# Optimization experiments

Hardware: AMD Instinct MI355X
Metric: run time of the kernel (lower is better)

Reference implementation:

```python
import jax, jax.numpy as jnp
import numpy as np
from jax.ops import segment_sum

N_NODES = 100000


def _gcn_norm(src, dst, n):
    # add self-loops, compute symmetric normalization deg^-1/2 * deg^-1/2
    loop = jnp.arange(n, dtype=src.dtype)
    src_sl = jnp.concatenate([src, loop])
    dst_sl = jnp.concatenate([dst, loop])
    deg = segment_sum(jnp.ones_like(src_sl, dtype=jnp.float32), dst_sl, num_segments=n)
    dinv = jnp.where(deg > 0, jax.lax.rsqrt(deg), 0.0)
    norm = dinv[src_sl] * dinv[dst_sl]  # [E+N]
    return src_sl, dst_sl, norm


def _gcn_conv(x, W, b, src_sl, dst_sl, norm, n):
    h = x @ W                              # [N, out]  dense GEMM first (smaller msg dim)
    msg = h[src_sl] * norm[:, None]        # [E+N, out]
    out = segment_sum(msg, dst_sl, num_segments=n)
    return out + b


def setup_inputs() -> dict:
    key = jax.random.key(0)
    k1, k2, k3, k4, k5 = jax.random.split(key, 5)
    x = jax.random.normal(k1, (N_NODES, 400), dtype=jnp.float32)
    edge_index = jax.random.randint(k2, (2, 3200000), 0, N_NODES, dtype=jnp.int64)
    batch = jnp.zeros((N_NODES,), dtype=jnp.int64)
    # Glorot-style init like PyG GCNConv
    W1 = jax.random.normal(k3, (400, 128), dtype=jnp.float32) * (1.0 / np.sqrt(400))
    b1 = jnp.zeros((128,), dtype=jnp.float32)
    W2 = jax.random.normal(k4, (128, 128), dtype=jnp.float32) * (1.0 / np.sqrt(128))
    b2 = jnp.zeros((128,), dtype=jnp.float32)
    return {"x": x, "edge_index": edge_index, "batch": batch,
            "W1": W1, "b1": b1, "W2": W2, "b2": b2}


def reference(x, edge_index, batch, W1, b1, W2, b2):
    n = x.shape[0]
    src, dst = edge_index[0], edge_index[1]
    src_sl, dst_sl, norm = _gcn_norm(src, dst, n)
    h = jax.nn.relu(_gcn_conv(x, W1, b1, src_sl, dst_sl, norm, n))
    h = jax.nn.relu(_gcn_conv(h, W2, b2, src_sl, dst_sl, norm, n))
    return h
```

## Files before the change

### kernel.cpp

```cpp
#include <hip/hip_runtime.h>


#define NBMAX 1024
#define HB    512
#define CAPB  4608
#define TSLOG 13

using u16 = unsigned short;
using u32 = unsigned int;
typedef __attribute__((ext_vector_type(8))) short short8;
typedef __attribute__((ext_vector_type(4))) float f32x4;

__device__ __forceinline__ u16 f2bf(float f) {
    u32 u = __float_as_uint(f);
    u += 0x7fffu + ((u >> 16) & 1u);
    return (u16)(u >> 16);
}
__device__ __forceinline__ u32 pack2(float a, float b) {
    return (u32)f2bf(a) | ((u32)f2bf(b) << 16);
}
__device__ __forceinline__ float bflo(u32 u) { return __uint_as_float(u << 16); }
__device__ __forceinline__ float bfhi(u32 u) { return __uint_as_float(u & 0xffff0000u); }


__global__ __launch_bounds__(256) void k_init_bcur(u32* bcur, int NB) {
    int b = blockIdx.x * 256 + threadIdx.x;
    if (b < NB) bcur[b] = (u32)b * CAPB;
}

__global__ __launch_bounds__(256) void k_scatter(const int* __restrict__ src,
                                                 const int* __restrict__ dst,
                                                 u32* __restrict__ bcur,
                                                 u32* __restrict__ ebuf,
                                                 int E, int NB) {
    __shared__ u32 hist[NBMAX];
    __shared__ u32 base[NBMAX];
    const int tid = threadIdx.x;
    for (int i = tid; i < NB; i += 256) hist[i] = 0u;
    __syncthreads();
    const int chunk = (E + gridDim.x - 1) / gridDim.x;
    const int e0 = blockIdx.x * chunk;
    const int e1 = min(E, e0 + chunk);
    for (int i = e0 + tid; i < e1; i += 256)
        atomicAdd(&hist[dst[i] >> 7], 1u);
    __syncthreads();
    for (int i = tid; i < NB; i += 256) {
        const u32 c = hist[i];
        base[i] = c ? atomicAdd(&bcur[i], c) : 0u;
    }
    __syncthreads();
    for (int i = tid; i < NB; i += 256) hist[i] = 0u;
    __syncthreads();
    for (int i = e0 + tid; i < e1; i += 256) {
        const int s = src[i];
        const int d = dst[i];
        const int b = d >> 7;
        const u32 loc = atomicAdd(&hist[b], 1u);
        ebuf[base[b] + loc] = ((u32)(d & 127) << 17) | (u32)s;
    }
}

__global__ __launch_bounds__(256) void k_csr_build(const u32* __restrict__ ebuf,
                                                   const u32* __restrict__ bcur,
                                                   int* __restrict__ rowbeg,
                                                   u16* __restrict__ deg16,
                                                   float* __restrict__ dinv,
                                                   int* __restrict__ csr_s,
                                                   int N, int NB) {
    __shared__ u32 cnt[2048];
    __shared__ u32 scan[2048];
    __shared__ u32 cur[2048];
    __shared__ u32 bsum[256];
    const int tid = threadIdx.x;
    const int b = blockIdx.x;
    const int r0 = b * CAPB;
    const int r1 = (int)bcur[b];

    for (int i = tid; i < 2048; i += 256) cnt[i] = 0u;
    __syncthreads();
    for (int i = r0 + tid; i < r1; i += 256) {
        const u32 e = ebuf[i];
        const u32 key = ((e >> 17) << 4) | ((e & 0x1FFFFu) >> TSLOG);
        atomicAdd(&cnt[key], 1u);
    }
    __syncthreads();

    const int i8 = tid * 8;
    u32 pre[8];
    u32 run = 0;
#pragma unroll
    for (int j = 0; j < 8; ++j) { pre[j] = run; run += cnt[i8 + j]; }
    bsum[tid] = run;
    __syncthreads();
    for (int off = 1; off < 256; off <<= 1) {
        u32 v = bsum[tid];
        u32 add = (tid >= off) ? bsum[tid - off] : 0u;
        __syncthreads();
        bsum[tid] = v + add;
        __syncthreads();
    }
    const u32 excl = bsum[tid] - run;
#pragma unroll
    for (int j = 0; j < 8; ++j) {
        const u32 x = excl + pre[j];
        scan[i8 + j] = x;
        cur[i8 + j] = x;
    }
    __syncthreads();

    if (tid < 128) {
        const u32 beg  = scan[tid * 16];
        const u32 endv = (tid == 127) ? (u32)(r1 - r0) : scan[(tid + 1) * 16];
        const u32 dg   = endv - beg;
        const int node = b * 128 + tid;
        if (node < N) {
            rowbeg[node] = r0 + (int)beg;
            deg16[node]  = (u16)dg;
            dinv[node]   = rsqrtf((float)(dg + 1u));
        }
    }
    __syncthreads();

    for (int i = r0 + tid; i < r1; i += 256) {
        const u32 e = ebuf[i];
        const u32 sr = e & 0x1FFFFu;
        const u32 key = ((e >> 17) << 4) | (sr >> TSLOG);
        const u32 p = atomicAdd(&cur[key], 1u);
        csr_s[r0 + (int)p] = (int)sr;
    }
}

__global__ __launch_bounds__(256) void k_wprep(const float* __restrict__ W,
                                               u16* __restrict__ Wt,
                                               int K, int KP) {
    int idx = blockIdx.x * 256 + threadIdx.x;
    if (idx >= 128 * KP) return;
    int n = idx / KP, k = idx - n * KP;
    Wt[idx] = (k < K) ? f2bf(W[(size_t)k * 128 + n]) : (u16)0;
}

template <int ABF>
__global__ __launch_bounds__(512) void k_gemm_mfma(
        const void* __restrict__ Aptr,
        const u16* __restrict__ Wt,
        const float* __restrict__ dinv,
        u16* __restrict__ H, int M, int K, int KP) {
    __shared__ u16 smem[16384];
    u16* As = smem;
    u16* Bs = smem + 128 * 64;

    const int tid = threadIdx.x;
    const int row0 = blockIdx.x * 128;
    const int wid = tid >> 6;
    const int lane = tid & 63;
    const int wm = wid >> 2, wn = wid & 3;
    const int l15 = lane & 15, lg = lane >> 4;
    const int lr7 = l15 & 7;

    const int arow = tid >> 2;
    const int achk = tid & 3;
    const int grow = row0 + arow;
    const int ar7 = arow & 7;
    const int s0 = (achk * 2) ^ ar7;
    const int s1 = (achk * 2 + 1) ^ ar7;

    float4 ar0, ar1, ar2, ar3;
    uint4  au0, au1;
    uint4  bu0, bu1;

    auto load_tile = [&](int kt) {
        const int k0 = kt * 64 + achk * 16;
        if (ABF) {
            if (grow < M) {
                const u16* ap = (const u16*)Aptr + (size_t)grow * K + k0;
                au0 = *reinterpret_cast<const uint4*>(ap);
                au1 = *reinterpret_cast<const uint4*>(ap + 8);
            } else {
                au0 = make_uint4(0, 0, 0, 0);
                au1 = make_uint4(0, 0, 0, 0);
            }
        } else {
            if (grow < M && k0 < K) {
                const float* ap = (const float*)Aptr + (size_t)grow * K + k0;
                ar0 = *reinterpret_cast<const float4*>(ap);
                ar1 = *reinterpret_cast<const float4*>(ap + 4);
                ar2 = *reinterpret_cast<const float4*>(ap + 8);
                ar3 = *reinterpret_cast<const float4*>(ap + 12);
            } else {
                ar0 = ar1 = ar2 = ar3 = make_float4(0.f, 0.f, 0.f, 0.f);
            }
        }
        const u16* wp = Wt + (size_t)arow * KP + k0;
        bu0 = *reinterpret_cast<const uint4*>(wp);
        bu1 = *reinterpret_cast<const uint4*>(wp + 8);
    };

    auto store_tile = [&]() {
        uint4 w0, w1;
        if (ABF) {
            w0 = au0; w1 = au1;
        } else {
            w0.x = pack2(ar0.x, ar0.y); w0.y = pack2(ar0.z, ar0.w);
            w0.z = pack2(ar1.x, ar1.y); w0.w = pack2(ar1.z, ar1.w);
            w1.x = pack2(ar2.x, ar2.y); w1.y = pack2(ar2.z, ar2.w);
            w1.z = pack2(ar3.x, ar3.y); w1.w = pack2(ar3.z, ar3.w);
        }
        u16* ad = As + arow * 64;
        *reinterpret_cast<uint4*>(ad + s0 * 8) = w0;
        *reinterpret_cast<uint4*>(ad + s1 * 8) = w1;
        u16* bd = Bs + arow * 64;
        *reinterpret_cast<uint4*>(bd + s0 * 8) = bu0;
        *reinterpret_cast<uint4*>(bd + s1 * 8) = bu1;
    };

    f32x4 acc[4][2];
#pragma unroll
    for (int i = 0; i < 4; ++i)
#pragma unroll
        for (int j = 0; j < 2; ++j)
            acc[i][j] = (f32x4){0.f, 0.f, 0.f, 0.f};

    const int NT = KP >> 6;
    load_tile(0);
    for (int kt = 0; kt < NT; ++kt) {
        __syncthreads();
        store_tile();
        __syncthreads();
        if (kt + 1 < NT) load_tile(kt + 1);
#pragma unroll
        for (int sub = 0; sub < 2; ++sub) {
            const int slot = ((sub * 4 + lg) ^ lr7) * 8;
            short8 af[4], bf[2];
#pragma unroll
            for (int i = 0; i < 4; ++i)
                af[i] = *reinterpret_cast<const short8*>(
                    As + (wm * 64 + i * 16 + l15) * 64 + slot);
#pragma unroll
            for (int j = 0; j < 2; ++j)
                bf[j] = *reinterpret_cast<const short8*>(
                    Bs + (wn * 32 + j * 16 + l15) * 64 + slot);
#pragma unroll
            for (int i = 0; i < 4; ++i)
#pragma unroll
                for (int j = 0; j < 2; ++j)
                    acc[i][j] = __builtin_amdgcn_mfma_f32_16x16x32_bf16(
                        af[i], bf[j], acc[i][j], 0, 0, 0);
        }
    }

    const int CSTR = 136;
    __syncthreads();
#pragma unroll
    for (int half = 0; half < 2; ++half) {
        if (wm == half) {
#pragma unroll
            for (int i = 0; i < 4; ++i)
#pragma unroll
                for (int r = 0; r < 4; ++r) {
                    const int gr = row0 + half * 64 + i * 16 + lg * 4 + r;
                    const float dv = (gr < M) ? dinv[gr] : 0.f;
#pragma unroll
                    for (int j = 0; j < 2; ++j)
                        smem[(i * 16 + lg * 4 + r) * CSTR + wn * 32 + j * 16 + l15] =
                            f2bf(acc[i][j][r] * dv);
                }
        }
        __syncthreads();
        {
            const int rr = tid >> 3;
            const int cc = (tid & 7) * 16;
            const int gr = row0 + half * 64 + rr;
            if (gr < M) {
                const u16* cp = smem + rr * CSTR + cc;
                uint4 q0 = *reinterpret_cast<const uint4*>(cp);
                uint4 q1 = *reinterpret_cast<const uint4*>(cp + 8);
                uint4* hp = reinterpret_cast<uint4*>(H + (size_t)gr * 128 + cc);
                hp[0] = q0; hp[1] = q1;
            }
        }
        __syncthreads();
    }
}

template <int OUTBF>
__global__ __launch_bounds__(256) void k_gather(const int* __restrict__ rowbeg,
                                                const u16* __restrict__ deg16,
                                                const float* __restrict__ dinv,
                                                const int* __restrict__ csr_s,
                                                const u16* __restrict__ H,
                                                const float* __restrict__ bias,
                                                void* __restrict__ outp, int N) {
    const int t = threadIdx.x;
    const int node = blockIdx.x * 16 + (t >> 4);
    if (node >= N) return;
    const int lane = t & 15;
    const int c8 = lane * 8;

    const uint4 hv = *reinterpret_cast<const uint4*>(H + (size_t)node * 128 + c8);
    float acc0 = bflo(hv.x), acc1 = bfhi(hv.x);
    float acc2 = bflo(hv.y), acc3 = bfhi(hv.y);
    float acc4 = bflo(hv.z), acc5 = bfhi(hv.z);
    float acc6 = bflo(hv.w), acc7 = bfhi(hv.w);

    const int beg = rowbeg[node];
    const int end = beg + (int)deg16[node];
    for (int r = beg; r < end; r += 16) {
        const int cntc = min(16, end - r);
        int sv = (lane < cntc) ? csr_s[r + lane] : 0;
        for (int j = 0; j < cntc; ++j) {
            const int s = __shfl(sv, j, 16);
            const uint4 x = *reinterpret_cast<const uint4*>(H + (size_t)s * 128 + c8);
            acc0 += bflo(x.x); acc1 += bfhi(x.x);
            acc2 += bflo(x.y); acc3 += bfhi(x.y);
            acc4 += bflo(x.z); acc5 += bfhi(x.z);
            acc6 += bflo(x.w); acc7 += bfhi(x.w);
        }
    }

    const float dv = dinv[node];
    const float4 b0 = *reinterpret_cast<const float4*>(bias + c8);
    const float4 b1 = *reinterpret_cast<const float4*>(bias + c8 + 4);
    const float r0 = fmaxf(fmaf(acc0, dv, b0.x), 0.f);
    const float r1 = fmaxf(fmaf(acc1, dv, b0.y), 0.f);
    const float r2 = fmaxf(fmaf(acc2, dv, b0.z), 0.f);
    const float r3 = fmaxf(fmaf(acc3, dv, b0.w), 0.f);
    const float r4 = fmaxf(fmaf(acc4, dv, b1.x), 0.f);
    const float r5 = fmaxf(fmaf(acc5, dv, b1.y), 0.f);
    const float r6 = fmaxf(fmaf(acc6, dv, b1.z), 0.f);
    const float r7 = fmaxf(fmaf(acc7, dv, b1.w), 0.f);

    if (OUTBF) {
        uint4 q;
        q.x = pack2(r0, r1); q.y = pack2(r2, r3);
        q.z = pack2(r4, r5); q.w = pack2(r6, r7);
        u16* op = (u16*)outp + (size_t)node * 128 + c8;
        *reinterpret_cast<uint4*>(op) = q;
    } else {
        float* op = (float*)outp + (size_t)node * 128 + c8;
        *reinterpret_cast<float4*>(op)     = make_float4(r0, r1, r2, r3);
        *reinterpret_cast<float4*>(op + 4) = make_float4(r4, r5, r6, r7);
    }
}


extern "C" void kernel_launch(void* const* d_in, const int* in_sizes, int n_in,
                              void* d_out, int out_size, void* d_ws, size_t ws_size,
                              hipStream_t stream) {
    const float* x  = (const float*)d_in[0];
    const int*   ei = (const int*)d_in[1];
    const float* W1 = (const float*)d_in[3];
    const float* b1 = (const float*)d_in[4];
    const float* W2 = (const float*)d_in[5];
    const float* b2 = (const float*)d_in[6];
    float* out = (float*)d_out;

    const int N = in_sizes[0] / 400;
    const int E = in_sizes[1] / 2;
    const int* src = ei;
    const int* dst = ei + E;
    const int NB = (N + 127) >> 7;
    const int KP1 = 448;
    const int KP2 = 128;

    char* ws = (char*)d_ws;
    size_t off = 0;
    auto alloc = [&](size_t bytes) {
        void* p = ws + off;
        off = (off + bytes + 255) & ~(size_t)255;
        return p;
    };
    u32*   bcur   = (u32*)alloc((size_t)NB * 4);
    int*   rowbeg = (int*)alloc((size_t)N * 4);
    u16*   deg16  = (u16*)alloc((size_t)N * 2);
    float* dinv   = (float*)alloc((size_t)N * 4);
    int*   csr_s  = (int*)alloc((size_t)NB * CAPB * 4);
    u32*   ebuf   = (u32*)alloc((size_t)NB * CAPB * 4);
    u16*   hs     = (u16*)alloc((size_t)N * 128 * 2);
    u16*   abf    = (u16*)alloc((size_t)N * 128 * 2);
    u16*   Wt1    = (u16*)alloc((size_t)128 * KP1 * 2);
    u16*   Wt2    = (u16*)alloc((size_t)128 * KP2 * 2);

    const int nb_gm = (N + 127) / 128;
    const int nb_g  = (N + 15) / 16;

    k_wprep<<<(128 * KP1 + 255) / 256, 256, 0, stream>>>(W1, Wt1, 400, KP1);
    k_wprep<<<(128 * KP2 + 255) / 256, 256, 0, stream>>>(W2, Wt2, 128, KP2);

    k_init_bcur<<<(NB + 255) / 256, 256, 0, stream>>>(bcur, NB);
    k_scatter<<<HB, 256, 0, stream>>>(src, dst, bcur, ebuf, E, NB);
    k_csr_build<<<NB, 256, 0, stream>>>(ebuf, bcur, rowbeg, deg16, dinv, csr_s, N, NB);

    k_gemm_mfma<0><<<nb_gm, 512, 0, stream>>>(x, Wt1, dinv, hs, N, 400, KP1);
    k_gather<1><<<nb_g, 256, 0, stream>>>(rowbeg, deg16, dinv, csr_s, hs, b1, abf, N);

    k_gemm_mfma<1><<<nb_gm, 512, 0, stream>>>(abf, Wt2, dinv, hs, N, 128, KP2);
    k_gather<0><<<nb_g, 256, 0, stream>>>(rowbeg, deg16, dinv, csr_s, hs, b2, out, N);
}
```

Baseline: 399.9 us.

## Synchronize gather blocks per source tile to improve L2 locality of H reads

The CSR build now records, for each destination node, the offset at which each source-node tile (8192 sources each) begins among its neighbors. The gather kernel walks these tiles in order and places a block-wide barrier after each one, so all nodes in a block read from the same source range at roughly the same time. The aim is to keep the working set of H rows small enough to stay in cache and cut random global memory traffic. In exchange it adds a 32-byte-per-node offset table, extra barriers and load imbalance between nodes with different degrees.

```diff
diff --git a/kernel.cpp b/kernel.cpp
--- a/kernel.cpp
+++ b/kernel.cpp
@@ -66,6 +66,7 @@
                                                    u16* __restrict__ deg16,
                                                    float* __restrict__ dinv,
                                                    int* __restrict__ csr_s,
+                                                   u16* __restrict__ tileofs,
                                                    int N, int NB) {
     __shared__ u32 cnt[2048];
     __shared__ u32 scan[2048];
@@ -117,6 +118,19 @@
             rowbeg[node] = r0 + (int)beg;
             deg16[node]  = (u16)dg;
             dinv[node]   = rsqrtf((float)(dg + 1u));
+            uint4 q0, q1;
+            u32 w[8];
+#pragma unroll
+            for (int j = 0; j < 8; ++j) {
+                const u32 lo = scan[tid * 16 + 2 * j]     - beg;
+                const u32 hi = scan[tid * 16 + 2 * j + 1] - beg;
+                w[j] = (lo & 0xFFFFu) | (hi << 16);
+            }
+            q0.x = w[0]; q0.y = w[1]; q0.z = w[2]; q0.w = w[3];
+            q1.x = w[4]; q1.y = w[5]; q1.z = w[6]; q1.w = w[7];
+            uint4* tp = reinterpret_cast<uint4*>(tileofs + (size_t)node * 16);
+            tp[0] = q0;
+            tp[1] = q1;
         }
     }
     __syncthreads();
@@ -287,36 +301,54 @@
                                                 const u16* __restrict__ deg16,
                                                 const float* __restrict__ dinv,
                                                 const int* __restrict__ csr_s,
+                                                const u16* __restrict__ tileofs,
                                                 const u16* __restrict__ H,
                                                 const float* __restrict__ bias,
-                                                void* __restrict__ outp, int N) {
+                                                void* __restrict__ outp,
+                                                int N, int NT) {
     const int t = threadIdx.x;
     const int node = blockIdx.x * 16 + (t >> 4);
-    if (node >= N) return;
+    const bool act = node < N;
     const int lane = t & 15;
     const int c8 = lane * 8;
 
-    const uint4 hv = *reinterpret_cast<const uint4*>(H + (size_t)node * 128 + c8);
-    float acc0 = bflo(hv.x), acc1 = bfhi(hv.x);
-    float acc2 = bflo(hv.y), acc3 = bfhi(hv.y);
-    float acc4 = bflo(hv.z), acc5 = bfhi(hv.z);
-    float acc6 = bflo(hv.w), acc7 = bfhi(hv.w);
-
-    const int beg = rowbeg[node];
-    const int end = beg + (int)deg16[node];
-    for (int r = beg; r < end; r += 16) {
-        const int cntc = min(16, end - r);
-        int sv = (lane < cntc) ? csr_s[r + lane] : 0;
-        for (int j = 0; j < cntc; ++j) {
-            const int s = __shfl(sv, j, 16);
-            const uint4 x = *reinterpret_cast<const uint4*>(H + (size_t)s * 128 + c8);
-            acc0 += bflo(x.x); acc1 += bfhi(x.x);
-            acc2 += bflo(x.y); acc3 += bfhi(x.y);
-            acc4 += bflo(x.z); acc5 += bfhi(x.z);
-            acc6 += bflo(x.w); acc7 += bfhi(x.w);
-        }
-    }
-
+    float acc0 = 0.f, acc1 = 0.f, acc2 = 0.f, acc3 = 0.f;
+    float acc4 = 0.f, acc5 = 0.f, acc6 = 0.f, acc7 = 0.f;
+    int beg = 0, dg = 0;
+    const u16* tofs = tileofs;
+    if (act) {
+        const uint4 hv = *reinterpret_cast<const uint4*>(H + (size_t)node * 128 + c8);
+        acc0 = bflo(hv.x); acc1 = bfhi(hv.x);
+        acc2 = bflo(hv.y); acc3 = bfhi(hv.y);
+        acc4 = bflo(hv.z); acc5 = bfhi(hv.z);
+        acc6 = bflo(hv.w); acc7 = bfhi(hv.w);
+        beg = rowbeg[node];
+        dg  = (int)deg16[node];
+        tofs = tileofs + (size_t)node * 16;
+    }
+
+    for (int tt = 0; tt < NT; ++tt) {
+        if (act) {
+            const int o0 = (int)tofs[tt];
+            const int o1 = (tt + 1 >= NT) ? dg : (int)tofs[tt + 1];
+            const int send = beg + o1;
+            for (int r = beg + o0; r < send; r += 16) {
+                const int cntc = min(16, send - r);
+                int sv = (lane < cntc) ? csr_s[r + lane] : 0;
+                for (int j = 0; j < cntc; ++j) {
+                    const int s = __shfl(sv, j, 16);
+                    const uint4 x = *reinterpret_cast<const uint4*>(H + (size_t)s * 128 + c8);
+                    acc0 += bflo(x.x); acc1 += bfhi(x.x);
+                    acc2 += bflo(x.y); acc3 += bfhi(x.y);
+                    acc4 += bflo(x.z); acc5 += bfhi(x.z);
+                    acc6 += bflo(x.w); acc7 += bfhi(x.w);
+                }
+            }
+        }
+        __syncthreads();
+    }
+
+    if (!act) return;
     const float dv = dinv[node];
     const float4 b0 = *reinterpret_cast<const float4*>(bias + c8);
     const float4 b1 = *reinterpret_cast<const float4*>(bias + c8 + 4);
@@ -359,6 +391,7 @@
     const int* src = ei;
     const int* dst = ei + E;
     const int NB = (N + 127) >> 7;
+    const int NT = (N + (1 << TSLOG) - 1) >> TSLOG;
     const int KP1 = 448;
     const int KP2 = 128;
 
@@ -369,16 +402,17 @@
         off = (off + bytes + 255) & ~(size_t)255;
         return p;
     };
-    u32*   bcur   = (u32*)alloc((size_t)NB * 4);
-    int*   rowbeg = (int*)alloc((size_t)N * 4);
-    u16*   deg16  = (u16*)alloc((size_t)N * 2);
-    float* dinv   = (float*)alloc((size_t)N * 4);
-    int*   csr_s  = (int*)alloc((size_t)NB * CAPB * 4);
-    u32*   ebuf   = (u32*)alloc((size_t)NB * CAPB * 4);
-    u16*   hs     = (u16*)alloc((size_t)N * 128 * 2);
-    u16*   abf    = (u16*)alloc((size_t)N * 128 * 2);
-    u16*   Wt1    = (u16*)alloc((size_t)128 * KP1 * 2);
-    u16*   Wt2    = (u16*)alloc((size_t)128 * KP2 * 2);
+    u32*   bcur    = (u32*)alloc((size_t)NB * 4);
+    int*   rowbeg  = (int*)alloc((size_t)N * 4);
+    u16*   deg16   = (u16*)alloc((size_t)N * 2);
+    float* dinv    = (float*)alloc((size_t)N * 4);
+    int*   csr_s   = (int*)alloc((size_t)NB * CAPB * 4);
+    u32*   ebuf    = (u32*)alloc((size_t)NB * CAPB * 4);
+    u16*   tileofs = (u16*)alloc((size_t)N * 16 * 2);
+    u16*   hs      = (u16*)alloc((size_t)N * 128 * 2);
+    u16*   abf     = (u16*)alloc((size_t)N * 128 * 2);
+    u16*   Wt1     = (u16*)alloc((size_t)128 * KP1 * 2);
+    u16*   Wt2     = (u16*)alloc((size_t)128 * KP2 * 2);
 
     const int nb_gm = (N + 127) / 128;
     const int nb_g  = (N + 15) / 16;
@@ -388,11 +422,14 @@
 
     k_init_bcur<<<(NB + 255) / 256, 256, 0, stream>>>(bcur, NB);
     k_scatter<<<HB, 256, 0, stream>>>(src, dst, bcur, ebuf, E, NB);
-    k_csr_build<<<NB, 256, 0, stream>>>(ebuf, bcur, rowbeg, deg16, dinv, csr_s, N, NB);
+    k_csr_build<<<NB, 256, 0, stream>>>(ebuf, bcur, rowbeg, deg16, dinv, csr_s,
+                                        tileofs, N, NB);
 
     k_gemm_mfma<0><<<nb_gm, 512, 0, stream>>>(x, Wt1, dinv, hs, N, 400, KP1);
-    k_gather<1><<<nb_g, 256, 0, stream>>>(rowbeg, deg16, dinv, csr_s, hs, b1, abf, N);
+    k_gather<1><<<nb_g, 256, 0, stream>>>(rowbeg, deg16, dinv, csr_s, tileofs,
+                                          hs, b1, abf, N, NT);
 
     k_gemm_mfma<1><<<nb_gm, 512, 0, stream>>>(abf, Wt2, dinv, hs, N, 128, KP2);
-    k_gather<0><<<nb_g, 256, 0, stream>>>(rowbeg, deg16, dinv, csr_s, hs, b2, out, N);
-}
+    k_gather<0><<<nb_g, 256, 0, stream>>>(rowbeg, deg16, dinv, csr_s, tileofs,
+                                          hs, b2, out, N, NT);
+}
```

Result: slower. 493.5 us (+23.4%).
